# Kernel tuning notes

Measured on AMD Instinct MI355X. Metric: run time of the kernel, lower is better.

## Reference

```python
import jax, jax.numpy as jnp
import numpy as np

B, T, M, E, H, D = 4, 1024, 1024, 1024, 16, 64
SCALE = D ** (-0.5)


def setup_inputs() -> dict:
    key = jax.random.key(0)
    ks = jax.random.split(key, 8)
    w = 0.02  # weight scale for numerical stability of softmax
    return {
        "x": jax.random.normal(ks[0], (B, T, E), jnp.float32),
        "xl_memory": jax.random.normal(ks[1], (B, M, 2, H * D), jnp.float32),
        "relative_positions": jax.random.normal(ks[2], (H, T, M + T), jnp.float32),
        "Wq": jax.random.normal(ks[3], (E, H * D), jnp.float32) * w,
        "bq": jnp.zeros((H * D,), jnp.float32),
        "Wk": jax.random.normal(ks[4], (E, H * D), jnp.float32) * w,
        "bk": jnp.zeros((H * D,), jnp.float32),
        "Wv": jax.random.normal(ks[5], (E, H * D), jnp.float32) * w,
        "bv": jnp.zeros((H * D,), jnp.float32),
        "Wo": jax.random.normal(ks[6], (H * D, E), jnp.float32) * w,
        "bo": jnp.zeros((E,), jnp.float32),
    }


def reference(x, xl_memory, relative_positions, Wq, bq, Wk, bk, Wv, bv, Wo, bo):
    b, t, _ = x.shape
    q = (x @ Wq + bq) * SCALE                     # [b, t, H*D] (scale applied to queries)
    k = x @ Wk + bk
    v = x @ Wv + bv
    k_xl = xl_memory[:, :, 0]                      # [b, m, H*D]
    v_xl = xl_memory[:, :, 1]
    m = k_xl.shape[1]
    keys = jnp.concatenate((k_xl, k), axis=1)      # [b, j, H*D], j = m + t
    values = jnp.concatenate((v_xl, v), axis=1)
    j = keys.shape[1]

    qh = q.reshape(b, t, H, D).transpose(0, 2, 1, 3)       # b h i d
    kh = keys.reshape(b, j, H, D).transpose(0, 2, 1, 3)    # b h j d
    vh = values.reshape(b, j, H, D).transpose(0, 2, 1, 3)  # b h j d

    qk = jnp.einsum("bhid,bhjd->bhij", qh, kh)
    qk = relative_positions[..., -t:, -j:] + qk
    qk = qk * SCALE                                # second scale, faithful to source
    mask = jnp.triu(jnp.ones((t, j), dtype=bool), j - t + 1)
    qk = jnp.where(mask, -jnp.inf, qk)
    attn = jax.nn.softmax(qk, axis=-1)             # dropout p=0.0 -> identity

    qkv = jnp.einsum("bhij,bhjd->bhid", attn, vh)
    qkv = qkv.transpose(0, 2, 1, 3).reshape(b, t, H * D)
    out = qkv @ Wo + bo

    kv_memories = jnp.stack((keys, values), axis=-2)  # [b, j, 2, H*D]
    kv_to_add_xl = kv_memories[:, -m:]                 # [b, m, 2, H*D]
    return out, kv_to_add_xl
```

## Files before the change

kernel.cpp:

```cpp
#include <hip/hip_runtime.h>
#include <hip/hip_bf16.h>

typedef unsigned short u16;
typedef unsigned int u32;
typedef __attribute__((ext_vector_type(8))) short short8;
typedef __attribute__((ext_vector_type(4))) float f32x4;

#define B_ 4
#define T_ 1024
#define E_ 1024
#define NH 16
#define HD 1024
#define JTOT 2048
#define SCALE 0.125f
#define LOG2E 1.44269504f

__device__ __forceinline__ u16 f2b(float f) {
  u32 x = __float_as_uint(f);
  u32 r = (x + 0x7fffu + ((x >> 16) & 1u)) >> 16;
  return (u16)r;
}
__device__ __forceinline__ u16 f2b_fast(float f) {
  return (u16)((__float_as_uint(f) + 0x8000u) >> 16);
}
__device__ __forceinline__ float b2f(u16 b) {
  return __uint_as_float((u32)b << 16);
}
__device__ __forceinline__ float fexp2(float x) {
  float r;
  asm("v_exp_f32 %0, %1" : "=v"(r) : "v"(x));
  return r;
}
__device__ __forceinline__ u32 cvtpk(float lo, float hi) {
  u32 r;
  asm("v_cvt_pk_bf16_f32 %0, %1, %2" : "=v"(r) : "v"(lo), "v"(hi));
  return r;
}

__device__ __forceinline__ void gload_lds16(const void* g, void* l) {
  __builtin_amdgcn_global_load_lds((const __attribute__((address_space(1))) u32*)g,
                                   (__attribute__((address_space(3))) u32*)l, 16, 0, 0);
}

__device__ __forceinline__ short8 pack8(float4 f0, float4 f1) {
  short8 o;
  o[0] = (short)f2b(f0.x); o[1] = (short)f2b(f0.y);
  o[2] = (short)f2b(f0.z); o[3] = (short)f2b(f0.w);
  o[4] = (short)f2b(f1.x); o[5] = (short)f2b(f1.y);
  o[6] = (short)f2b(f1.z); o[7] = (short)f2b(f1.w);
  return o;
}

__global__ __launch_bounds__(256) void cvt_bf16(const float* __restrict__ in,
                                                u16* __restrict__ out, int n8) {
  int i = blockIdx.x * 256 + threadIdx.x;
  if (i >= n8) return;
  const float4* p = (const float4*)in + (size_t)i * 2;
  ((short8*)out)[i] = pack8(p[0], p[1]);
}

__global__ __launch_bounds__(256) void cvt_w4T(const float* __restrict__ Wq, const float* __restrict__ Wk,
                                               const float* __restrict__ Wv, const float* __restrict__ Wo,
                                               u16* __restrict__ wqkvT, u16* __restrict__ woT) {
  __shared__ float tile[64][65];
  const float* W;
  u16* WT;
  int z = blockIdx.z;
  if (z == 0) { W = Wq; WT = wqkvT; }
  else if (z == 1) { W = Wk; WT = wqkvT + (size_t)1024 * 1024; }
  else if (z == 2) { W = Wv; WT = wqkvT + (size_t)2048 * 1024; }
  else { W = Wo; WT = woT; }
  int t = threadIdx.x;
  int r0 = blockIdx.y * 64, c0 = blockIdx.x * 64;
#pragma unroll
  for (int i = 0; i < 16; ++i) {
    int r = i * 4 + (t >> 6), c = t & 63;
    tile[r][c] = W[(size_t)(r0 + r) * 1024 + c0 + c];
  }
  __syncthreads();
#pragma unroll
  for (int i = 0; i < 16; ++i) {
    int r = i * 4 + (t >> 6), c = t & 63;
    WT[(size_t)(c0 + r) * 1024 + r0 + c] = f2b(tile[c][r]);
  }
}

__global__ __launch_bounds__(256) void cvt_xl_k(const float* __restrict__ xl, u16* __restrict__ kt) {
  int i = blockIdx.x * 256 + threadIdx.x;
  int hd8 = i & 127, j = (i >> 7) & 1023, b = i >> 17;
  const float4* p = (const float4*)(xl + ((((size_t)b * 1024 + j) * 2 + 0) * 1024 + (size_t)hd8 * 8));
  short8 o = pack8(p[0], p[1]);
  int h = hd8 >> 3, d0 = (hd8 & 7) * 8;
  int jc = j >> 6, jl = j & 63;
  u16* dst = kt + (((size_t)(b * 16 + h) * 32 + jc) * 4096) + jl * 64 + (d0 ^ ((jl & 7) << 3));
  *(short8*)dst = o;
}

__global__ __launch_bounds__(256) void cvt_xl_vT(const float* __restrict__ xl, u16* __restrict__ vt) {
  __shared__ u16 Vl[64 * 72];
  int bx = blockIdx.x;
  int jc = bx & 15, h = (bx >> 4) & 15, b = bx >> 8;
  int t = threadIdx.x;
  int j0 = jc * 64;
#pragma unroll
  for (int it = 0; it < 2; ++it) {
    int p = t + 256 * it;
    int j = p >> 3, d8 = p & 7;
    const float4* src = (const float4*)(xl + ((((size_t)b * 1024 + j0 + j) * 2 + 1) * 1024 + h * 64 + (size_t)d8 * 8));
    *(short8*)&Vl[j * 72 + d8 * 8] = pack8(src[0], src[1]);
  }
  __syncthreads();
#pragma unroll
  for (int it = 0; it < 2; ++it) {
    int p = t + 256 * it;
    int d = p >> 3, j8 = p & 7;
    short8 o;
#pragma unroll
    for (int e = 0; e < 8; ++e) o[e] = (short)Vl[(j8 * 8 + e) * 72 + d];
    u16* dst = vt + (((size_t)(b * 16 + h) * 32 + jc) * 4096) + d * 64 + ((j8 * 8) ^ ((d & 7) << 3));
    *(short8*)dst = o;
  }
}

__global__ __launch_bounds__(256) void trans_vnew(const u16* __restrict__ vb, u16* __restrict__ vt) {
  __shared__ u16 Vl[64 * 72];
  int bx = blockIdx.x;
  int jcl = bx & 15, h = (bx >> 4) & 15, b = bx >> 8;
  int jc = 16 + jcl;
  int t = threadIdx.x;
  int t0 = jcl * 64;
#pragma unroll
  for (int it = 0; it < 2; ++it) {
    int p = t + 256 * it;
    int j = p >> 3, d8 = p & 7;
    *(short8*)&Vl[j * 72 + d8 * 8] =
        *(const short8*)&vb[((size_t)b * 1024 + t0 + j) * 1024 + h * 64 + d8 * 8];
  }
  __syncthreads();
#pragma unroll
  for (int it = 0; it < 2; ++it) {
    int p = t + 256 * it;
    int d = p >> 3, j8 = p & 7;
    short8 o;
#pragma unroll
    for (int e = 0; e < 8; ++e) o[e] = (short)Vl[(j8 * 8 + e) * 72 + d];
    u16* dst = vt + (((size_t)(b * 16 + h) * 32 + jc) * 4096) + d * 64 + ((j8 * 8) ^ ((d & 7) << 3));
    *(short8*)dst = o;
  }
}

__global__ __launch_bounds__(256) void gemm_qkv(
    const u16* __restrict__ A, const u16* __restrict__ BT,
    const float* __restrict__ b0, const float* __restrict__ b1, const float* __restrict__ b2,
    u16* __restrict__ qb, u16* __restrict__ kbp, u16* __restrict__ vb) {
  __shared__ __align__(16) u16 As[128 * 32];
  __shared__ __align__(16) u16 Bs[128 * 32];
  const int t = threadIdx.x;
  const int lane = t & 63, wv = t >> 6;
  const int wr = wv >> 1, wc = wv & 1;
  const int xcd = blockIdx.x & 7, loc = blockIdx.x >> 3;
  const int m0 = (loc / 3) * 128;
  const int n0 = (xcd * 3 + loc % 3) * 128;
  const int lr = lane & 15, lg = lane >> 4;

  f32x4 acc[4][4] = {};

  for (int kc = 0; kc < 1024; kc += 32) {
    __syncthreads();
#pragma unroll
    for (int i = 0; i < 2; ++i) {
      int p = t + 256 * i;
      gload_lds16(A + (size_t)(m0 + (p >> 2)) * 1024 + kc + (p & 3) * 8, &As[p * 8]);
    }
#pragma unroll
    for (int i = 0; i < 2; ++i) {
      int p = t + 256 * i;
      gload_lds16(BT + (size_t)(n0 + (p >> 2)) * 1024 + kc + (p & 3) * 8, &Bs[p * 8]);
    }
    __syncthreads();

    short8 af[4], bf[4];
#pragma unroll
    for (int mf = 0; mf < 4; ++mf)
      af[mf] = *(const short8*)&As[(wr * 64 + mf * 16 + lr) * 32 + lg * 8];
#pragma unroll
    for (int nf = 0; nf < 4; ++nf)
      bf[nf] = *(const short8*)&Bs[(wc * 64 + nf * 16 + lr) * 32 + lg * 8];
#pragma unroll
    for (int mf = 0; mf < 4; ++mf)
#pragma unroll
      for (int nf = 0; nf < 4; ++nf)
        acc[mf][nf] = __builtin_amdgcn_mfma_f32_16x16x32_bf16(af[mf], bf[nf], acc[mf][nf], 0, 0, 0);
  }

#pragma unroll
  for (int mf = 0; mf < 4; ++mf) {
#pragma unroll
    for (int nf = 0; nf < 4; ++nf) {
#pragma unroll
      for (int r = 0; r < 4; ++r) {
        int row = m0 + wr * 64 + mf * 16 + lg * 4 + r;
        int col = n0 + wc * 64 + nf * 16 + lr;
        float v = acc[mf][nf][r];
        int b = row >> 10, tt = row & 1023;
        if (col < 1024) {
          qb[(size_t)row * HD + col] = f2b((v + b0[col]) * (SCALE * SCALE * LOG2E));
        } else if (col < 2048) {
          int hd = col - 1024;
          kbp[(size_t)(b * 1024 + tt) * 1024 + hd] = f2b(v + b1[hd]);
        } else {
          int hd = col - 2048;
          vb[(size_t)(b * 1024 + tt) * 1024 + hd] = f2b(v + b2[hd]);
        }
      }
    }
  }
}

__global__ __launch_bounds__(256) void kv_expand(const u16* __restrict__ kbp, const u16* __restrict__ vbp,
                                                 float* __restrict__ kvout, u16* __restrict__ kt) {
  int i = blockIdx.x * 256 + threadIdx.x;
  int hd8 = i & 127, tt = (i >> 7) & 1023, b = i >> 17;
  size_t src = ((size_t)(b * 1024 + tt)) * 1024 + (size_t)hd8 * 8;
  short8 k8 = *(const short8*)&kbp[src];
  short8 v8 = *(const short8*)&vbp[src];
  float4 k0, k1, v0, v1;
#pragma unroll
  for (int e = 0; e < 4; ++e) {
    ((float*)&k0)[e] = b2f((u16)k8[e]); ((float*)&k1)[e] = b2f((u16)k8[e + 4]);
    ((float*)&v0)[e] = b2f((u16)v8[e]); ((float*)&v1)[e] = b2f((u16)v8[e + 4]);
  }
  float* kdst = kvout + (((size_t)(b * 1024 + tt) * 2 + 0) * 1024) + hd8 * 8;
  float* vdst = kvout + (((size_t)(b * 1024 + tt) * 2 + 1) * 1024) + hd8 * 8;
  ((float4*)kdst)[0] = k0; ((float4*)kdst)[1] = k1;
  ((float4*)vdst)[0] = v0; ((float4*)vdst)[1] = v1;
  int h = hd8 >> 3, d0 = (hd8 & 7) * 8;
  int jc = 16 + (tt >> 6), jl = tt & 63;
  u16* ktdst = kt + (((size_t)(b * 16 + h) * 32 + jc) * 4096) + jl * 64 + (d0 ^ ((jl & 7) << 3));
  *(short8*)ktdst = k8;
}

__global__ __launch_bounds__(256) void gemm_out(
    const u16* __restrict__ A, const u16* __restrict__ BT,
    const float* __restrict__ bias, float* __restrict__ outf) {
  __shared__ __align__(16) u16 As[64 * 32];
  __shared__ __align__(16) u16 Bs[128 * 32];
  const int t = threadIdx.x;
  const int lane = t & 63, wv = t >> 6;
  const int wr = wv >> 1, wc = wv & 1;
  const int m0 = (blockIdx.x >> 3) * 64;
  const int n0 = (blockIdx.x & 7) * 128;
  const int lr = lane & 15, lg = lane >> 4;

  f32x4 acc[2][4] = {};

  for (int kc = 0; kc < 1024; kc += 32) {
    __syncthreads();
    gload_lds16(A + (size_t)(m0 + (t >> 2)) * 1024 + kc + (t & 3) * 8, &As[t * 8]);
#pragma unroll
    for (int i = 0; i < 2; ++i) {
      int p = t + 256 * i;
      gload_lds16(BT + (size_t)(n0 + (p >> 2)) * 1024 + kc + (p & 3) * 8, &Bs[p * 8]);
    }
    __syncthreads();

    short8 af[2], bf[4];
#pragma unroll
    for (int mf = 0; mf < 2; ++mf)
      af[mf] = *(const short8*)&As[(wr * 32 + mf * 16 + lr) * 32 + lg * 8];
#pragma unroll
    for (int nf = 0; nf < 4; ++nf)
      bf[nf] = *(const short8*)&Bs[(wc * 64 + nf * 16 + lr) * 32 + lg * 8];
#pragma unroll
    for (int mf = 0; mf < 2; ++mf)
#pragma unroll
      for (int nf = 0; nf < 4; ++nf)
        acc[mf][nf] = __builtin_amdgcn_mfma_f32_16x16x32_bf16(af[mf], bf[nf], acc[mf][nf], 0, 0, 0);
  }

#pragma unroll
  for (int mf = 0; mf < 2; ++mf)
#pragma unroll
    for (int nf = 0; nf < 4; ++nf)
#pragma unroll
      for (int r = 0; r < 4; ++r) {
        int row = m0 + wr * 32 + mf * 16 + lg * 4 + r;
        int col = n0 + wc * 64 + nf * 16 + lr;
        outf[(size_t)row * E_ + col] = acc[mf][nf][r] + bias[col];
      }
}

__global__ __launch_bounds__(256) void attn_kernel(
    const u16* __restrict__ qb, const u16* __restrict__ kt, const u16* __restrict__ vt,
    const float* __restrict__ rel, u16* __restrict__ aout) {
  __shared__ __align__(16) u16 Ks[2][4096];
  __shared__ __align__(16) u16 Vs[2][4096];
  __shared__ __align__(16) u16 Pl[4096];
  const int bx = blockIdx.x;
  const int xcd = bx & 7, s = bx >> 3;
  const int b = s & 3, key = (s >> 2) * 8 + xcd;
  const int h = key & 15, qt = key >> 4;
  const int i0 = qt * 64;
  const int t = threadIdx.x, lane = t & 63, w = t >> 6;
  const int lr = lane & 15, lg = lane >> 4;
  const int swz = (lr & 7) << 3;
  const float RC = SCALE * LOG2E;

  const u16* ktb = kt + (size_t)(b * 16 + h) * 32 * 4096;
  const u16* vtb = vt + (size_t)(b * 16 + h) * 32 * 4096;
  const float* relrow = rel + (size_t)h * T_ * JTOT + (size_t)(i0 + w * 16 + lr) * JTOT + lg * 4;
  const int nch = qt + 17;

  short8 qf[2];
#pragma unroll
  for (int kc = 0; kc < 2; ++kc)
    qf[kc] = *(const short8*)&qb[(size_t)(b * T_ + i0 + w * 16 + lr) * HD + h * 64 + kc * 32 + lg * 8];

  short8 vf5;
#pragma unroll
  for (int e = 0; e < 8; ++e) vf5[e] = (lr == 0) ? (short)0x3f80 : (short)0;

  auto stage = [&](int buf, int jc2) {
    const u16* ksrc = ktb + (size_t)jc2 * 4096;
    const u16* vsrc = vtb + (size_t)jc2 * 4096;
    gload_lds16(ksrc + t * 8, &Ks[buf][t * 8]);
    gload_lds16(ksrc + (t + 256) * 8, &Ks[buf][(t + 256) * 8]);
    gload_lds16(vsrc + t * 8, &Vs[buf][t * 8]);
    gload_lds16(vsrc + (t + 256) * 8, &Vs[buf][(t + 256) * 8]);
  };

  auto loadrel = [&](int j0, float4 (&rlf)[4]) {
#pragma unroll
    for (int nf = 0; nf < 4; ++nf)
      rlf[nf] = *(const float4*)(relrow + j0 + nf * 16);
  };

  float4 rlA[4], rlB[4];
  stage(0, 0);
  __builtin_amdgcn_sched_barrier(0);
  loadrel(0, rlA);
  loadrel(64, rlB);

  f32x4 o[4] = {};
  f32x4 o5 = {};
  float mrow = -__builtin_inff();

  int cur = 0;
  auto chunkfn = [&](int jc, float4 (&rlu)[4]) {
    asm volatile("s_waitcnt vmcnt(4)" ::: "memory");
    __builtin_amdgcn_sched_barrier(0);
    asm volatile("s_barrier" ::: "memory");
    if (jc + 1 < nch) stage(cur ^ 1, jc + 1);
    __builtin_amdgcn_sched_barrier(0);

    f32x4 s4[4] = {};
#pragma unroll
    for (int nf = 0; nf < 4; ++nf)
#pragma unroll
      for (int kc = 0; kc < 2; ++kc) {
        short8 kf = *(const short8*)&Ks[cur][(nf * 16 + lr) * 64 + ((kc * 32 + lg * 8) ^ swz)];
        s4[nf] = __builtin_amdgcn_mfma_f32_16x16x32_bf16(kf, qf[kc], s4[nf], 0, 0, 0);
      }

    float p[4][4], lmax = -__builtin_inff();
    const bool domask = (jc == qt + 16);
#pragma unroll
    for (int nf = 0; nf < 4; ++nf)
#pragma unroll
      for (int r = 0; r < 4; ++r) {
        float v = fmaf(((const float*)&rlu[nf])[r], RC, s4[nf][r]);
        if (domask && (nf * 16 + lg * 4 + r) > (w * 16 + lr)) v = -__builtin_inff();
        p[nf][r] = v;
        lmax = fmaxf(lmax, v);
      }
    if (jc + 2 < nch) loadrel((jc + 2) * 64, rlu);

    const bool dores = !__all(lmax - mrow <= 11.0f);
    if (dores) {
      float ch = fmaxf(lmax, __shfl_xor(lmax, 16, 64));
      ch = fmaxf(ch, __shfl_xor(ch, 32, 64));
      float nm = fmaxf(mrow, ch);
      float sc = fexp2(mrow - nm);
      mrow = nm;
      float sco[4];
#pragma unroll
      for (int r = 0; r < 4; ++r) sco[r] = __shfl(sc, lg * 4 + r, 64);
#pragma unroll
      for (int nf = 0; nf < 4; ++nf)
#pragma unroll
        for (int r = 0; r < 4; ++r) o[nf][r] *= sco[r];
#pragma unroll
      for (int r = 0; r < 4; ++r) o5[r] *= sco[r];
    }

    {
      u32* plrow = (u32*)&Pl[(w * 16 + lr) * 64];
#pragma unroll
      for (int nf = 0; nf < 4; ++nf) {
        float e0 = fexp2(p[nf][0] - mrow), e1 = fexp2(p[nf][1] - mrow);
        float e2 = fexp2(p[nf][2] - mrow), e3 = fexp2(p[nf][3] - mrow);
        u32 w0 = cvtpk(e0, e1), w1 = cvtpk(e2, e3);
        plrow[((nf * 16 + lg * 4 + 0) ^ swz) >> 1] = w0;
        plrow[((nf * 16 + lg * 4 + 2) ^ swz) >> 1] = w1;
      }
    }

#pragma unroll
    for (int kc = 0; kc < 2; ++kc) {
      short8 pa = *(const short8*)&Pl[(w * 16 + lr) * 64 + ((kc * 32 + lg * 8) ^ swz)];
#pragma unroll
      for (int nf = 0; nf < 4; ++nf) {
        short8 vf = *(const short8*)&Vs[cur][(nf * 16 + lr) * 64 + ((kc * 32 + lg * 8) ^ swz)];
        o[nf] = __builtin_amdgcn_mfma_f32_16x16x32_bf16(pa, vf, o[nf], 0, 0, 0);
      }
      o5 = __builtin_amdgcn_mfma_f32_16x16x32_bf16(pa, vf5, o5, 0, 0, 0);
    }
    cur ^= 1;
  };

  int jc = 0;
  for (; jc + 1 < nch; jc += 2) {
    chunkfn(jc, rlA);
    chunkfn(jc + 1, rlB);
  }
  if (jc < nch) chunkfn(jc, rlA);

  float inv[4];
#pragma unroll
  for (int r = 0; r < 4; ++r)
    inv[r] = 1.0f / __shfl(o5[r], lane & 48, 64);
#pragma unroll
  for (int nf = 0; nf < 4; ++nf)
#pragma unroll
    for (int r = 0; r < 4; ++r) {
      int i = i0 + w * 16 + lg * 4 + r, d = nf * 16 + lr;
      aout[(size_t)(b * T_ + i) * HD + h * 64 + d] = f2b_fast(o[nf][r] * inv[r]);
    }
}

extern "C" void kernel_launch(void* const* d_in, const int* in_sizes, int n_in,
                              void* d_out, int out_size, void* d_ws, size_t ws_size,
                              hipStream_t stream) {
  const float* x  = (const float*)d_in[0];
  const float* xl = (const float*)d_in[1];
  const float* rel = (const float*)d_in[2];
  const float* Wq = (const float*)d_in[3];
  const float* bq = (const float*)d_in[4];
  const float* Wk = (const float*)d_in[5];
  const float* bk = (const float*)d_in[6];
  const float* Wv = (const float*)d_in[7];
  const float* bv = (const float*)d_in[8];
  const float* Wo = (const float*)d_in[9];
  const float* bo = (const float*)d_in[10];

  float* out = (float*)d_out;
  float* kvout = out + (size_t)B_ * T_ * E_;

  char* ws = (char*)d_ws;
  u16* xb    = (u16*)ws; ws += (size_t)4096 * 1024 * 2;
  u16* wqkvT = (u16*)ws; ws += (size_t)3072 * 1024 * 2;
  u16* woT   = (u16*)ws; ws += (size_t)1024 * 1024 * 2;
  u16* qbuf  = (u16*)ws; ws += (size_t)4096 * 1024 * 2;
  u16* kt    = (u16*)ws; ws += (size_t)B_ * NH * 32 * 4096 * 2;
  u16* vt    = (u16*)ws; ws += (size_t)B_ * NH * 32 * 4096 * 2;
  u16* vbn   = (u16*)ws; ws += (size_t)4096 * 1024 * 2;
  u16* kbp   = (u16*)ws; ws += (size_t)4096 * 1024 * 2;
  u16* aout  = (u16*)ws; ws += (size_t)4096 * 1024 * 2;

  cvt_bf16<<<2048, 256, 0, stream>>>(x, xb, 524288);
  cvt_w4T<<<dim3(16, 16, 4), 256, 0, stream>>>(Wq, Wk, Wv, Wo, wqkvT, woT);
  cvt_xl_k<<<2048, 256, 0, stream>>>(xl, kt);
  cvt_xl_vT<<<1024, 256, 0, stream>>>(xl, vt);

  gemm_qkv<<<768, 256, 0, stream>>>(xb, wqkvT, bq, bk, bv, qbuf, kbp, vbn);
  kv_expand<<<2048, 256, 0, stream>>>(kbp, vbn, kvout, kt);
  trans_vnew<<<1024, 256, 0, stream>>>(vbn, vt);
  attn_kernel<<<1024, 256, 0, stream>>>(qbuf, kt, vt, rel, aout);
  gemm_out<<<512, 256, 0, stream>>>(aout, woT, bo, out);
}
```

Measured before the change: 211.6 us.

## Split attention KV range across two wave groups and merge launches

The attention kernel now uses 512 threads per block: two groups of four waves each process half of the key chunks for the same 64 query rows. The partial outputs are merged through LDS with a log-sum-exp combine. The row sum is now accumulated with shuffles instead of an extra MFMA against a ones vector. The conversion kernels are fused into one launch, and kv_expand and trans_vnew are fused into another, to cut launch overhead. The trade-off is that double-buffered prefetch of K/V and the rel prefetch are dropped in favour of synchronous loads with two barriers per round, which may expose memory latency.

Result: slower. 291.2 us (+37.6%).

```diff
diff --git a/kernel.cpp b/kernel.cpp
--- a/kernel.cpp
+++ b/kernel.cpp
@@ -51,101 +51,72 @@
   return o;
 }
 
-__global__ __launch_bounds__(256) void cvt_bf16(const float* __restrict__ in,
-                                                u16* __restrict__ out, int n8) {
-  int i = blockIdx.x * 256 + threadIdx.x;
-  if (i >= n8) return;
-  const float4* p = (const float4*)in + (size_t)i * 2;
-  ((short8*)out)[i] = pack8(p[0], p[1]);
-}
-
-__global__ __launch_bounds__(256) void cvt_w4T(const float* __restrict__ Wq, const float* __restrict__ Wk,
-                                               const float* __restrict__ Wv, const float* __restrict__ Wo,
-                                               u16* __restrict__ wqkvT, u16* __restrict__ woT) {
-  __shared__ float tile[64][65];
-  const float* W;
-  u16* WT;
-  int z = blockIdx.z;
-  if (z == 0) { W = Wq; WT = wqkvT; }
-  else if (z == 1) { W = Wk; WT = wqkvT + (size_t)1024 * 1024; }
-  else if (z == 2) { W = Wv; WT = wqkvT + (size_t)2048 * 1024; }
-  else { W = Wo; WT = woT; }
-  int t = threadIdx.x;
-  int r0 = blockIdx.y * 64, c0 = blockIdx.x * 64;
-#pragma unroll
-  for (int i = 0; i < 16; ++i) {
-    int r = i * 4 + (t >> 6), c = t & 63;
-    tile[r][c] = W[(size_t)(r0 + r) * 1024 + c0 + c];
-  }
-  __syncthreads();
-#pragma unroll
-  for (int i = 0; i < 16; ++i) {
-    int r = i * 4 + (t >> 6), c = t & 63;
-    WT[(size_t)(c0 + r) * 1024 + r0 + c] = f2b(tile[c][r]);
-  }
-}
-
-__global__ __launch_bounds__(256) void cvt_xl_k(const float* __restrict__ xl, u16* __restrict__ kt) {
-  int i = blockIdx.x * 256 + threadIdx.x;
-  int hd8 = i & 127, j = (i >> 7) & 1023, b = i >> 17;
-  const float4* p = (const float4*)(xl + ((((size_t)b * 1024 + j) * 2 + 0) * 1024 + (size_t)hd8 * 8));
-  short8 o = pack8(p[0], p[1]);
-  int h = hd8 >> 3, d0 = (hd8 & 7) * 8;
-  int jc = j >> 6, jl = j & 63;
-  u16* dst = kt + (((size_t)(b * 16 + h) * 32 + jc) * 4096) + jl * 64 + (d0 ^ ((jl & 7) << 3));
-  *(short8*)dst = o;
-}
-
-__global__ __launch_bounds__(256) void cvt_xl_vT(const float* __restrict__ xl, u16* __restrict__ vt) {
-  __shared__ u16 Vl[64 * 72];
+__global__ __launch_bounds__(256) void cvt_all(
+    const float* __restrict__ x, const float* __restrict__ Wq, const float* __restrict__ Wk,
+    const float* __restrict__ Wv, const float* __restrict__ Wo, const float* __restrict__ xl,
+    u16* __restrict__ xb, u16* __restrict__ wqkvT, u16* __restrict__ woT,
+    u16* __restrict__ kt, u16* __restrict__ vt) {
   int bx = blockIdx.x;
-  int jc = bx & 15, h = (bx >> 4) & 15, b = bx >> 8;
-  int t = threadIdx.x;
-  int j0 = jc * 64;
-#pragma unroll
-  for (int it = 0; it < 2; ++it) {
-    int p = t + 256 * it;
-    int j = p >> 3, d8 = p & 7;
-    const float4* src = (const float4*)(xl + ((((size_t)b * 1024 + j0 + j) * 2 + 1) * 1024 + h * 64 + (size_t)d8 * 8));
-    *(short8*)&Vl[j * 72 + d8 * 8] = pack8(src[0], src[1]);
-  }
-  __syncthreads();
-#pragma unroll
-  for (int it = 0; it < 2; ++it) {
-    int p = t + 256 * it;
-    int d = p >> 3, j8 = p & 7;
-    short8 o;
-#pragma unroll
-    for (int e = 0; e < 8; ++e) o[e] = (short)Vl[(j8 * 8 + e) * 72 + d];
-    u16* dst = vt + (((size_t)(b * 16 + h) * 32 + jc) * 4096) + d * 64 + ((j8 * 8) ^ ((d & 7) << 3));
+  if (bx < 2048) {
+    int i = bx * 256 + threadIdx.x;
+    const float4* p = (const float4*)x + (size_t)i * 2;
+    ((short8*)xb)[i] = pack8(p[0], p[1]);
+  } else if (bx < 3072) {
+    __shared__ float tile[64][65];
+    int idx = bx - 2048;
+    int z = idx >> 8, yy = (idx >> 4) & 15, xx = idx & 15;
+    const float* W;
+    u16* WT;
+    if (z == 0) { W = Wq; WT = wqkvT; }
+    else if (z == 1) { W = Wk; WT = wqkvT + (size_t)1024 * 1024; }
+    else if (z == 2) { W = Wv; WT = wqkvT + (size_t)2048 * 1024; }
+    else { W = Wo; WT = woT; }
+    int t = threadIdx.x;
+    int r0 = yy * 64, c0 = xx * 64;
+#pragma unroll
+    for (int i = 0; i < 16; ++i) {
+      int r = i * 4 + (t >> 6), c = t & 63;
+      tile[r][c] = W[(size_t)(r0 + r) * 1024 + c0 + c];
+    }
+    __syncthreads();
+#pragma unroll
+    for (int i = 0; i < 16; ++i) {
+      int r = i * 4 + (t >> 6), c = t & 63;
+      WT[(size_t)(c0 + r) * 1024 + r0 + c] = f2b(tile[c][r]);
+    }
+  } else if (bx < 5120) {
+    int i = (bx - 3072) * 256 + threadIdx.x;
+    int hd8 = i & 127, j = (i >> 7) & 1023, b = i >> 17;
+    const float4* p = (const float4*)(xl + ((((size_t)b * 1024 + j) * 2 + 0) * 1024 + (size_t)hd8 * 8));
+    short8 o = pack8(p[0], p[1]);
+    int h = hd8 >> 3, d0 = (hd8 & 7) * 8;
+    int jc = j >> 6, jl = j & 63;
+    u16* dst = kt + (((size_t)(b * 16 + h) * 32 + jc) * 4096) + jl * 64 + (d0 ^ ((jl & 7) << 3));
     *(short8*)dst = o;
-  }
-}
-
-__global__ __launch_bounds__(256) void trans_vnew(const u16* __restrict__ vb, u16* __restrict__ vt) {
-  __shared__ u16 Vl[64 * 72];
-  int bx = blockIdx.x;
-  int jcl = bx & 15, h = (bx >> 4) & 15, b = bx >> 8;
-  int jc = 16 + jcl;
-  int t = threadIdx.x;
-  int t0 = jcl * 64;
-#pragma unroll
-  for (int it = 0; it < 2; ++it) {
-    int p = t + 256 * it;
-    int j = p >> 3, d8 = p & 7;
-    *(short8*)&Vl[j * 72 + d8 * 8] =
-        *(const short8*)&vb[((size_t)b * 1024 + t0 + j) * 1024 + h * 64 + d8 * 8];
-  }
-  __syncthreads();
-#pragma unroll
-  for (int it = 0; it < 2; ++it) {
-    int p = t + 256 * it;
-    int d = p >> 3, j8 = p & 7;
-    short8 o;
-#pragma unroll
-    for (int e = 0; e < 8; ++e) o[e] = (short)Vl[(j8 * 8 + e) * 72 + d];
-    u16* dst = vt + (((size_t)(b * 16 + h) * 32 + jc) * 4096) + d * 64 + ((j8 * 8) ^ ((d & 7) << 3));
-    *(short8*)dst = o;
+  } else {
+    __shared__ u16 Vl[64 * 72];
+    int bxx = bx - 5120;
+    int jc = bxx & 15, h = (bxx >> 4) & 15, b = bxx >> 8;
+    int t = threadIdx.x;
+    int j0 = jc * 64;
+#pragma unroll
+    for (int it = 0; it < 2; ++it) {
+      int p = t + 256 * it;
+      int j = p >> 3, d8 = p & 7;
+      const float4* src = (const float4*)(xl + ((((size_t)b * 1024 + j0 + j) * 2 + 1) * 1024 + h * 64 + (size_t)d8 * 8));
+      *(short8*)&Vl[j * 72 + d8 * 8] = pack8(src[0], src[1]);
+    }
+    __syncthreads();
+#pragma unroll
+    for (int it = 0; it < 2; ++it) {
+      int p = t + 256 * it;
+      int d = p >> 3, j8 = p & 7;
+      short8 o;
+#pragma unroll
+      for (int e = 0; e < 8; ++e) o[e] = (short)Vl[(j8 * 8 + e) * 72 + d];
+      u16* dst = vt + (((size_t)(b * 16 + h) * 32 + jc) * 4096) + d * 64 + ((j8 * 8) ^ ((d & 7) << 3));
+      *(short8*)dst = o;
+    }
   }
 }
 
@@ -217,27 +188,56 @@
   }
 }
 
-__global__ __launch_bounds__(256) void kv_expand(const u16* __restrict__ kbp, const u16* __restrict__ vbp,
-                                                 float* __restrict__ kvout, u16* __restrict__ kt) {
-  int i = blockIdx.x * 256 + threadIdx.x;
-  int hd8 = i & 127, tt = (i >> 7) & 1023, b = i >> 17;
-  size_t src = ((size_t)(b * 1024 + tt)) * 1024 + (size_t)hd8 * 8;
-  short8 k8 = *(const short8*)&kbp[src];
-  short8 v8 = *(const short8*)&vbp[src];
-  float4 k0, k1, v0, v1;
-#pragma unroll
-  for (int e = 0; e < 4; ++e) {
-    ((float*)&k0)[e] = b2f((u16)k8[e]); ((float*)&k1)[e] = b2f((u16)k8[e + 4]);
-    ((float*)&v0)[e] = b2f((u16)v8[e]); ((float*)&v1)[e] = b2f((u16)v8[e + 4]);
-  }
-  float* kdst = kvout + (((size_t)(b * 1024 + tt) * 2 + 0) * 1024) + hd8 * 8;
-  float* vdst = kvout + (((size_t)(b * 1024 + tt) * 2 + 1) * 1024) + hd8 * 8;
-  ((float4*)kdst)[0] = k0; ((float4*)kdst)[1] = k1;
-  ((float4*)vdst)[0] = v0; ((float4*)vdst)[1] = v1;
-  int h = hd8 >> 3, d0 = (hd8 & 7) * 8;
-  int jc = 16 + (tt >> 6), jl = tt & 63;
-  u16* ktdst = kt + (((size_t)(b * 16 + h) * 32 + jc) * 4096) + jl * 64 + (d0 ^ ((jl & 7) << 3));
-  *(short8*)ktdst = k8;
+__global__ __launch_bounds__(256) void post_gemm(const u16* __restrict__ kbp, const u16* __restrict__ vbp,
+                                                 float* __restrict__ kvout, u16* __restrict__ kt,
+                                                 u16* __restrict__ vt) {
+  int bx = blockIdx.x;
+  if (bx < 2048) {
+    int i = bx * 256 + threadIdx.x;
+    int hd8 = i & 127, tt = (i >> 7) & 1023, b = i >> 17;
+    size_t src = ((size_t)(b * 1024 + tt)) * 1024 + (size_t)hd8 * 8;
+    short8 k8 = *(const short8*)&kbp[src];
+    short8 v8 = *(const short8*)&vbp[src];
+    float4 k0, k1, v0, v1;
+#pragma unroll
+    for (int e = 0; e < 4; ++e) {
+      ((float*)&k0)[e] = b2f((u16)k8[e]); ((float*)&k1)[e] = b2f((u16)k8[e + 4]);
+      ((float*)&v0)[e] = b2f((u16)v8[e]); ((float*)&v1)[e] = b2f((u16)v8[e + 4]);
+    }
+    float* kdst = kvout + (((size_t)(b * 1024 + tt) * 2 + 0) * 1024) + hd8 * 8;
+    float* vdst = kvout + (((size_t)(b * 1024 + tt) * 2 + 1) * 1024) + hd8 * 8;
+    ((float4*)kdst)[0] = k0; ((float4*)kdst)[1] = k1;
+    ((float4*)vdst)[0] = v0; ((float4*)vdst)[1] = v1;
+    int h = hd8 >> 3, d0 = (hd8 & 7) * 8;
+    int jc = 16 + (tt >> 6), jl = tt & 63;
+    u16* ktdst = kt + (((size_t)(b * 16 + h) * 32 + jc) * 4096) + jl * 64 + (d0 ^ ((jl & 7) << 3));
+    *(short8*)ktdst = k8;
+  } else {
+    __shared__ u16 Vl[64 * 72];
+    int bxx = bx - 2048;
+    int jcl = bxx & 15, h = (bxx >> 4) & 15, b = bxx >> 8;
+    int jc = 16 + jcl;
+    int t = threadIdx.x;
+    int t0 = jcl * 64;
+#pragma unroll
+    for (int it = 0; it < 2; ++it) {
+      int p = t + 256 * it;
+      int j = p >> 3, d8 = p & 7;
+      *(short8*)&Vl[j * 72 + d8 * 8] =
+          *(const short8*)&vbp[((size_t)b * 1024 + t0 + j) * 1024 + h * 64 + d8 * 8];
+    }
+    __syncthreads();
+#pragma unroll
+    for (int it = 0; it < 2; ++it) {
+      int p = t + 256 * it;
+      int d = p >> 3, j8 = p & 7;
+      short8 o;
+#pragma unroll
+      for (int e = 0; e < 8; ++e) o[e] = (short)Vl[(j8 * 8 + e) * 72 + d];
+      u16* dst = vt + (((size_t)(b * 16 + h) * 32 + jc) * 4096) + d * 64 + ((j8 * 8) ^ ((d & 7) << 3));
+      *(short8*)dst = o;
+    }
+  }
 }
 
 __global__ __launch_bounds__(256) void gemm_out(
@@ -290,75 +290,71 @@
       }
 }
 
-__global__ __launch_bounds__(256) void attn_kernel(
+__global__ __launch_bounds__(512, 6) void attn_kernel(
     const u16* __restrict__ qb, const u16* __restrict__ kt, const u16* __restrict__ vt,
     const float* __restrict__ rel, u16* __restrict__ aout) {
-  __shared__ __align__(16) u16 Ks[2][4096];
-  __shared__ __align__(16) u16 Vs[2][4096];
-  __shared__ __align__(16) u16 Pl[4096];
+  __shared__ __align__(16) u16 L[24576];
   const int bx = blockIdx.x;
   const int xcd = bx & 7, s = bx >> 3;
   const int b = s & 3, key = (s >> 2) * 8 + xcd;
   const int h = key & 15, qt = key >> 4;
   const int i0 = qt * 64;
-  const int t = threadIdx.x, lane = t & 63, w = t >> 6;
+  const int t = threadIdx.x, lane = t & 63, wv = t >> 6;
+  const int grp = wv >> 2, w4 = wv & 3, tg = t & 255;
   const int lr = lane & 15, lg = lane >> 4;
   const int swz = (lr & 7) << 3;
   const float RC = SCALE * LOG2E;
 
+  u16* Ks = L + grp * 12288;
+  u16* Vs = Ks + 4096;
+  u16* Pl = Vs + 4096;
+
   const u16* ktb = kt + (size_t)(b * 16 + h) * 32 * 4096;
   const u16* vtb = vt + (size_t)(b * 16 + h) * 32 * 4096;
-  const float* relrow = rel + (size_t)h * T_ * JTOT + (size_t)(i0 + w * 16 + lr) * JTOT + lg * 4;
+  const float* relrow = rel + (size_t)h * T_ * JTOT + (size_t)(i0 + w4 * 16 + lr) * JTOT + lg * 4;
+
   const int nch = qt + 17;
+  const int n0 = nch >> 1;
+  const int rounds = nch - n0;
+  const int jbase = grp ? n0 : 0;
+  const int jend = grp ? nch : n0;
 
   short8 qf[2];
 #pragma unroll
   for (int kc = 0; kc < 2; ++kc)
-    qf[kc] = *(const short8*)&qb[(size_t)(b * T_ + i0 + w * 16 + lr) * HD + h * 64 + kc * 32 + lg * 8];
-
-  short8 vf5;
-#pragma unroll
-  for (int e = 0; e < 8; ++e) vf5[e] = (lr == 0) ? (short)0x3f80 : (short)0;
-
-  auto stage = [&](int buf, int jc2) {
-    const u16* ksrc = ktb + (size_t)jc2 * 4096;
-    const u16* vsrc = vtb + (size_t)jc2 * 4096;
-    gload_lds16(ksrc + t * 8, &Ks[buf][t * 8]);
-    gload_lds16(ksrc + (t + 256) * 8, &Ks[buf][(t + 256) * 8]);
-    gload_lds16(vsrc + t * 8, &Vs[buf][t * 8]);
-    gload_lds16(vsrc + (t + 256) * 8, &Vs[buf][(t + 256) * 8]);
-  };
-
-  auto loadrel = [&](int j0, float4 (&rlf)[4]) {
-#pragma unroll
-    for (int nf = 0; nf < 4; ++nf)
-      rlf[nf] = *(const float4*)(relrow + j0 + nf * 16);
-  };
-
-  float4 rlA[4], rlB[4];
-  stage(0, 0);
-  __builtin_amdgcn_sched_barrier(0);
-  loadrel(0, rlA);
-  loadrel(64, rlB);
+    qf[kc] = *(const short8*)&qb[(size_t)(b * T_ + i0 + w4 * 16 + lr) * HD + h * 64 + kc * 32 + lg * 8];
 
   f32x4 o[4] = {};
-  f32x4 o5 = {};
-  float mrow = -__builtin_inff();
-
-  int cur = 0;
-  auto chunkfn = [&](int jc, float4 (&rlu)[4]) {
-    asm volatile("s_waitcnt vmcnt(4)" ::: "memory");
+  float lsum = 0.f, mrow = -__builtin_inff();
+
+  for (int rd = 0; rd < rounds; ++rd) {
+    const int jc = jbase + rd;
+    const bool act = (jc < jend);
+    asm volatile("s_barrier" ::: "memory");
+    if (act) {
+      const u16* ksrc = ktb + (size_t)jc * 4096;
+      const u16* vsrc = vtb + (size_t)jc * 4096;
+      gload_lds16(ksrc + tg * 8, Ks + tg * 8);
+      gload_lds16(ksrc + (tg + 256) * 8, Ks + (tg + 256) * 8);
+      gload_lds16(vsrc + tg * 8, Vs + tg * 8);
+      gload_lds16(vsrc + (tg + 256) * 8, Vs + (tg + 256) * 8);
+      asm volatile("s_waitcnt vmcnt(0)" ::: "memory");
+    }
     __builtin_amdgcn_sched_barrier(0);
     asm volatile("s_barrier" ::: "memory");
-    if (jc + 1 < nch) stage(cur ^ 1, jc + 1);
-    __builtin_amdgcn_sched_barrier(0);
+    if (!act) continue;
+
+    float4 rl[4];
+#pragma unroll
+    for (int nf = 0; nf < 4; ++nf)
+      rl[nf] = *(const float4*)(relrow + jc * 64 + nf * 16);
 
     f32x4 s4[4] = {};
 #pragma unroll
     for (int nf = 0; nf < 4; ++nf)
 #pragma unroll
       for (int kc = 0; kc < 2; ++kc) {
-        short8 kf = *(const short8*)&Ks[cur][(nf * 16 + lr) * 64 + ((kc * 32 + lg * 8) ^ swz)];
+        short8 kf = *(const short8*)&Ks[(nf * 16 + lr) * 64 + ((kc * 32 + lg * 8) ^ swz)];
         s4[nf] = __builtin_amdgcn_mfma_f32_16x16x32_bf16(kf, qf[kc], s4[nf], 0, 0, 0);
       }
 
@@ -368,12 +364,11 @@
     for (int nf = 0; nf < 4; ++nf)
 #pragma unroll
       for (int r = 0; r < 4; ++r) {
-        float v = fmaf(((const float*)&rlu[nf])[r], RC, s4[nf][r]);
-        if (domask && (nf * 16 + lg * 4 + r) > (w * 16 + lr)) v = -__builtin_inff();
+        float v = fmaf(((const float*)&rl[nf])[r], RC, s4[nf][r]);
+        if (domask && (nf * 16 + lg * 4 + r) > (w4 * 16 + lr)) v = -__builtin_inff();
         p[nf][r] = v;
         lmax = fmaxf(lmax, v);
       }
-    if (jc + 2 < nch) loadrel((jc + 2) * 64, rlu);
 
     const bool dores = !__all(lmax - mrow <= 11.0f);
     if (dores) {
@@ -382,6 +377,7 @@
       float nm = fmaxf(mrow, ch);
       float sc = fexp2(mrow - nm);
       mrow = nm;
+      lsum *= sc;
       float sco[4];
 #pragma unroll
       for (int r = 0; r < 4; ++r) sco[r] = __shfl(sc, lg * 4 + r, 64);
@@ -389,53 +385,70 @@
       for (int nf = 0; nf < 4; ++nf)
 #pragma unroll
         for (int r = 0; r < 4; ++r) o[nf][r] *= sco[r];
-#pragma unroll
-      for (int r = 0; r < 4; ++r) o5[r] *= sco[r];
-    }
-
+    }
+
+    float rs = 0.f;
     {
-      u32* plrow = (u32*)&Pl[(w * 16 + lr) * 64];
+      u32* plrow = (u32*)&Pl[(w4 * 16 + lr) * 64];
 #pragma unroll
       for (int nf = 0; nf < 4; ++nf) {
         float e0 = fexp2(p[nf][0] - mrow), e1 = fexp2(p[nf][1] - mrow);
         float e2 = fexp2(p[nf][2] - mrow), e3 = fexp2(p[nf][3] - mrow);
+        rs += (e0 + e1) + (e2 + e3);
         u32 w0 = cvtpk(e0, e1), w1 = cvtpk(e2, e3);
         plrow[((nf * 16 + lg * 4 + 0) ^ swz) >> 1] = w0;
         plrow[((nf * 16 + lg * 4 + 2) ^ swz) >> 1] = w1;
       }
     }
+    rs += __shfl_xor(rs, 16, 64);
+    rs += __shfl_xor(rs, 32, 64);
+    lsum += rs;
 
 #pragma unroll
     for (int kc = 0; kc < 2; ++kc) {
-      short8 pa = *(const short8*)&Pl[(w * 16 + lr) * 64 + ((kc * 32 + lg * 8) ^ swz)];
+      short8 pa = *(const short8*)&Pl[(w4 * 16 + lr) * 64 + ((kc * 32 + lg * 8) ^ swz)];
 #pragma unroll
       for (int nf = 0; nf < 4; ++nf) {
-        short8 vf = *(const short8*)&Vs[cur][(nf * 16 + lr) * 64 + ((kc * 32 + lg * 8) ^ swz)];
+        short8 vf = *(const short8*)&Vs[(nf * 16 + lr) * 64 + ((kc * 32 + lg * 8) ^ swz)];
         o[nf] = __builtin_amdgcn_mfma_f32_16x16x32_bf16(pa, vf, o[nf], 0, 0, 0);
       }
-      o5 = __builtin_amdgcn_mfma_f32_16x16x32_bf16(pa, vf5, o5, 0, 0, 0);
-    }
-    cur ^= 1;
-  };
-
-  int jc = 0;
-  for (; jc + 1 < nch; jc += 2) {
-    chunkfn(jc, rlA);
-    chunkfn(jc + 1, rlB);
-  }
-  if (jc < nch) chunkfn(jc, rlA);
-
-  float inv[4];
-#pragma unroll
-  for (int r = 0; r < 4; ++r)
-    inv[r] = 1.0f / __shfl(o5[r], lane & 48, 64);
-#pragma unroll
-  for (int nf = 0; nf < 4; ++nf)
+    }
+  }
+
+  __syncthreads();
+  float* mo = (float*)L;
+  float* ml = (float*)(L + 8192);
+  if (grp == 0) {
+#pragma unroll
+    for (int nf = 0; nf < 4; ++nf)
+#pragma unroll
+      for (int r = 0; r < 4; ++r)
+        mo[(w4 * 16 + lg * 4 + r) * 64 + nf * 16 + lr] = o[nf][r];
+    if (lg == 0) {
+      ml[w4 * 16 + lr] = mrow;
+      ml[64 + w4 * 16 + lr] = lsum;
+    }
+  }
+  __syncthreads();
+  if (grp == 1) {
+    float m1o[4], l1o[4];
 #pragma unroll
     for (int r = 0; r < 4; ++r) {
-      int i = i0 + w * 16 + lg * 4 + r, d = nf * 16 + lr;
-      aout[(size_t)(b * T_ + i) * HD + h * 64 + d] = f2b_fast(o[nf][r] * inv[r]);
-    }
+      m1o[r] = __shfl(mrow, lg * 4 + r, 64);
+      l1o[r] = __shfl(lsum, lg * 4 + r, 64);
+    }
+#pragma unroll
+    for (int nf = 0; nf < 4; ++nf)
+#pragma unroll
+      for (int r = 0; r < 4; ++r) {
+        int i = w4 * 16 + lg * 4 + r, d = nf * 16 + lr;
+        float m0v = ml[i], l0v = ml[64 + i];
+        float mm = fmaxf(m0v, m1o[r]);
+        float w0 = fexp2(m0v - mm), w1 = fexp2(m1o[r] - mm);
+        float outv = (mo[i * 64 + d] * w0 + o[nf][r] * w1) / (l0v * w0 + l1o[r] * w1);
+        aout[(size_t)(b * T_ + i0 + i) * HD + h * 64 + d] = f2b_fast(outv);
+      }
+  }
 }
 
 extern "C" void kernel_launch(void* const* d_in, const int* in_sizes, int n_in,
@@ -467,14 +480,9 @@
   u16* kbp   = (u16*)ws; ws += (size_t)4096 * 1024 * 2;
   u16* aout  = (u16*)ws; ws += (size_t)4096 * 1024 * 2;
 
-  cvt_bf16<<<2048, 256, 0, stream>>>(x, xb, 524288);
-  cvt_w4T<<<dim3(16, 16, 4), 256, 0, stream>>>(Wq, Wk, Wv, Wo, wqkvT, woT);
-  cvt_xl_k<<<2048, 256, 0, stream>>>(xl, kt);
-  cvt_xl_vT<<<1024, 256, 0, stream>>>(xl, vt);
-
+  cvt_all<<<6144, 256, 0, stream>>>(x, Wq, Wk, Wv, Wo, xl, xb, wqkvT, woT, kt, vt);
   gemm_qkv<<<768, 256, 0, stream>>>(xb, wqkvT, bq, bk, bv, qbuf, kbp, vbn);
-  kv_expand<<<2048, 256, 0, stream>>>(kbp, vbn, kvout, kt);
-  trans_vnew<<<1024, 256, 0, stream>>>(vbn, vt);
-  attn_kernel<<<1024, 256, 0, stream>>>(qbuf, kt, vt, rel, aout);
+  post_gemm<<<3072, 256, 0, stream>>>(kbp, vbn, kvout, kt, vt);
+  attn_kernel<<<1024, 512, 0, stream>>>(qbuf, kt, vt, rel, aout);
   gemm_out<<<512, 256, 0, stream>>>(aout, woT, bo, out);
 }
```
